# Kernel optimization log

Hardware: AMD Instinct MI355X
Metric: run time of the kernel (lower is better)

Reference implementation:

```python
import jax, jax.numpy as jnp
import numpy as np

N_POINTS = 1440   # number of detector angles (thetas)
N_INT = 4000      # trapezoid integration samples along each ray
N_GRID = 4096     # SoS field is (N_GRID, N_GRID)
GRID_LO, GRID_HI = -0.06, 0.06
R_BODY = 0.05
V0 = 1500.0


def setup_inputs() -> dict:
    key = jax.random.key(0)
    k1, k2, k3 = jax.random.split(key, 3)
    # query point strictly inside the body circle (r < R_body)
    x = jnp.float32(0.012)
    y = jnp.float32(-0.007)
    # speed-of-sound field ~ water SoS with heterogeneity, strictly positive
    SoS = (1480.0 + 40.0 * jax.random.uniform(k3, (N_GRID, N_GRID))).astype(jnp.float32)
    thetas = jnp.linspace(0.0, 2.0 * jnp.pi, N_POINTS, dtype=jnp.float32).reshape(-1, 1)
    steps = jnp.linspace(0.0, 1.0, N_INT, dtype=jnp.float32).reshape(1, -1)
    x_vec = jnp.linspace(GRID_LO, GRID_HI, N_GRID, dtype=jnp.float32)
    dx = x_vec[1] - x_vec[0]
    return {
        "x": x, "y": y, "SoS": SoS,
        "thetas": thetas, "steps": steps,
        "x0": x_vec[0], "y0": x_vec[0], "dx": dx, "dy": dx,
        "R_body": jnp.float32(R_BODY), "v0": jnp.float32(V0),
    }


def reference(x, y, SoS, thetas, steps, x0, y0, dx, dy, R_body, v0):
    # polar coords of query point; note torch code uses atan2(x, y)
    r = jnp.sqrt(x * x + y * y)
    phi = jnp.arctan2(x, y)
    s = r * jnp.sin(thetas - phi)                      # (P,1)
    arg = jnp.maximum(R_body * R_body - s * s, 0.0)    # shared, >0 when r<R_body
    sqrt_arg = jnp.sqrt(arg)
    l_in = sqrt_arg + r * jnp.cos(thetas - phi)
    l_out = 2.0 * sqrt_arg * (jnp.cos(phi - thetas) >= 0.0).astype(sqrt_arg.dtype)
    l = jnp.where(r < R_body, l_in, l_out)             # (P,1) chord lengths

    xs = l * steps                                     # (P,N) arc-length samples
    px = x - xs * jnp.sin(thetas)                      # (P,N) sample positions
    py = y - xs * jnp.cos(thetas)
    x_index = jnp.round((px - x0) / dx).astype(jnp.int32)
    y_index = jnp.round((py - y0) / dy).astype(jnp.int32)
    # gather: negative row index (-y_index) wraps from the end, as in torch/numpy
    vals = 1.0 - v0 / SoS[-y_index, x_index]           # (P,N)
    # trapezoid over non-uniformly labeled x = l*steps (uniform per row)
    dseg = jnp.diff(xs, axis=1)                        # (P,N-1)
    wf = jnp.sum(0.5 * (vals[:, :-1] + vals[:, 1:]) * dseg, axis=1)
    return thetas.reshape(-1), wf
```

## Files before the change

kernel.cpp:

```cpp
#include <hip/hip_runtime.h>

#define N_POINTS 1440
#define N_INT    4000
#define N_GRID   4096
#define BLOCK    256

#define NSEG     8
#define SEG_LEN  (N_INT / NSEG)
#define RPC      4
#define NCLUST   (N_POINTS / RPC)
#define QS       (BLOCK / RPC)
#define FULL_ITS (SEG_LEN / QS)
#define REM_Q    (SEG_LEN - FULL_ITS * QS)

__global__ __launch_bounds__(BLOCK, 8) void wavefront_partial_kernel(
    const float* __restrict__ xp,
    const float* __restrict__ yp,
    const float* __restrict__ SoS,
    const float* __restrict__ thetas,
    const float* __restrict__ x0p,
    const float* __restrict__ y0p,
    const float* __restrict__ dxp,
    const float* __restrict__ dyp,
    const float* __restrict__ Rp,
    const float* __restrict__ v0p,
    float* __restrict__ ws)
{
    const int b = blockIdx.x;
    const int j = b >> 3;
    const int S = ((b & 7) + j) & 7;
    const int t = threadIdx.x;
    const int r = t & 3;
    const int q = t >> 2;

    const int p = j * RPC + r;

    const float x  = xp[0];
    const float y  = yp[0];
    const float x0 = x0p[0];
    const float y0 = y0p[0];
    const float dx = dxp[0];
    const float dy = dyp[0];
    const float Rb = Rp[0];
    const float v0 = v0p[0];

    const float theta = thetas[p];

    const float rr  = sqrtf(x * x + y * y);
    const float phi = atan2f(x, y);
    const float st  = sinf(theta);
    const float ct  = cosf(theta);

    const float sv    = rr * sinf(theta - phi);
    const float arg   = fmaxf(Rb * Rb - sv * sv, 0.0f);
    const float sq    = sqrtf(arg);
    const float l_in  = sq + rr * cosf(theta - phi);
    const float l_out = 2.0f * sq * (cosf(phi - theta) >= 0.0f ? 1.0f : 0.0f);
    const float l     = (rr < Rb) ? l_in : l_out;

    const float ds = 1.0f / 3999.0f;
    const float Ax = (x - x0) / dx;
    const float Bx = l * st / dx;
    const float Ay = (y - y0) / dy;
    const float By = l * ct / dy;

    const int   jb     = S * SEG_LEN + q;
    const float s_base = (float)jb * ds;
    const float fx0  = fmaf(-Bx, s_base, Ax);
    const float fy0  = fmaf(-By, s_base, Ay);
    const float nBxd = -Bx * ((float)QS * ds);
    const float nByd = -By * ((float)QS * ds);

    float acc;

#define SAMPLE(itf, vdst)                                            \
    {                                                                \
        const float fx = fmaf((itf), nBxd, fx0);                     \
        const float fy = fmaf((itf), nByd, fy0);                     \
        const int xi = (int)rintf(fx);                               \
        const int yi = (int)rintf(fy);                               \
        const int idx = ((N_GRID - yi) << 12) + xi;                  \
        const float sosv = SoS[idx];                                 \
        vdst = fmaf(-v0, __builtin_amdgcn_rcpf(sosv), 1.0f);         \
    }

    { float v; SAMPLE(0.0f, v); if (S == 0 && q == 0) v *= 0.5f; acc = v; }
#pragma unroll
    for (int it = 1; it < FULL_ITS; ++it) {
        float v; SAMPLE((float)it, v); acc += v;
    }
    if (q < REM_Q) {
        float v; SAMPLE((float)FULL_ITS, v);
        if (S == NSEG - 1 && q == REM_Q - 1) v *= 0.5f;
        acc += v;
    }
#undef SAMPLE

    acc += __shfl_xor(acc, 4, 64);
    acc += __shfl_xor(acc, 8, 64);
    acc += __shfl_xor(acc, 16, 64);
    acc += __shfl_xor(acc, 32, 64);

    __shared__ float wsum[4][4];
    if ((t & 63) < 4) wsum[t >> 6][r] = acc;
    __syncthreads();
    if (t < 4) {
        const float tot = (wsum[0][t] + wsum[1][t]) + (wsum[2][t] + wsum[3][t]);
        ws[(j * RPC + t) * NSEG + S] = tot;
    }
}

__global__ __launch_bounds__(BLOCK) void wavefront_combine_kernel(
    const float* __restrict__ xp,
    const float* __restrict__ yp,
    const float* __restrict__ thetas,
    const float* __restrict__ Rp,
    const float* __restrict__ ws,
    float* __restrict__ out)
{
    const int p = blockIdx.x * BLOCK + threadIdx.x;
    if (p >= N_POINTS) return;

    const float x  = xp[0];
    const float y  = yp[0];
    const float Rb = Rp[0];
    const float theta = thetas[p];

    const float rr  = sqrtf(x * x + y * y);
    const float phi = atan2f(x, y);
    const float sv    = rr * sinf(theta - phi);
    const float arg   = fmaxf(Rb * Rb - sv * sv, 0.0f);
    const float sq    = sqrtf(arg);
    const float l_in  = sq + rr * cosf(theta - phi);
    const float l_out = 2.0f * sq * (cosf(phi - theta) >= 0.0f ? 1.0f : 0.0f);
    const float l     = (rr < Rb) ? l_in : l_out;

    const float4* w4 = (const float4*)(ws + p * NSEG);
    const float4 a = w4[0], b4 = w4[1];
    const float tot = ((a.x + a.y) + (a.z + a.w)) + ((b4.x + b4.y) + (b4.z + b4.w));

    out[p] = theta;
    out[N_POINTS + p] = l * (1.0f / 3999.0f) * tot;
}

extern "C" void kernel_launch(void* const* d_in, const int* in_sizes, int n_in,
                              void* d_out, int out_size, void* d_ws, size_t ws_size,
                              hipStream_t stream) {
    (void)in_sizes; (void)n_in; (void)out_size; (void)ws_size;

    const float* xp     = (const float*)d_in[0];
    const float* yp     = (const float*)d_in[1];
    const float* SoS    = (const float*)d_in[2];
    const float* thetas = (const float*)d_in[3];
    const float* x0p    = (const float*)d_in[5];
    const float* y0p    = (const float*)d_in[6];
    const float* dxp    = (const float*)d_in[7];
    const float* dyp    = (const float*)d_in[8];
    const float* Rp     = (const float*)d_in[9];
    const float* v0p    = (const float*)d_in[10];

    float* ws  = (float*)d_ws;
    float* out = (float*)d_out;

    wavefront_partial_kernel<<<NCLUST * NSEG, BLOCK, 0, stream>>>(
        xp, yp, SoS, thetas, x0p, y0p, dxp, dyp, Rp, v0p, ws);
    wavefront_combine_kernel<<<(N_POINTS + BLOCK - 1) / BLOCK, BLOCK, 0, stream>>>(
        xp, yp, thetas, Rp, ws, out);
}
```

Baseline: 119.8 us.

## Halve segments, batch gathers before reciprocals, and hoist the v0 multiply

Each block now covers a quarter of a ray instead of an eighth, so each thread issues about 16 gathers. All SoS loads go out first into a register array, and only then are reciprocals taken, which raises memory-level parallelism per thread. Rounding is folded into biased truncation. The 1 - v0/s term is rewritten as n - v0*sum(1/s), with the trapezoid endpoint halving applied as a correction. The trade-off is fewer blocks and more registers (occupancy hint lowered from 8 to 6 blocks), plus slight numeric differences from reassociation and truncation instead of rintf.

```diff
diff --git a/kernel.cpp b/kernel.cpp
--- a/kernel.cpp
+++ b/kernel.cpp
@@ -5,15 +5,14 @@
 #define N_GRID   4096
 #define BLOCK    256
 
-#define NSEG     8
+#define NSEG     4
 #define SEG_LEN  (N_INT / NSEG)
 #define RPC      4
 #define NCLUST   (N_POINTS / RPC)
-#define QS       (BLOCK / RPC)
-#define FULL_ITS (SEG_LEN / QS)
-#define REM_Q    (SEG_LEN - FULL_ITS * QS)
+#define K_FULL   15
+#define TAIL_Q   (SEG_LEN - K_FULL * 64)
 
-__global__ __launch_bounds__(BLOCK, 8) void wavefront_partial_kernel(
+__global__ __launch_bounds__(BLOCK, 6) void wavefront_partial_kernel(
     const float* __restrict__ xp,
     const float* __restrict__ yp,
     const float* __restrict__ SoS,
@@ -27,13 +26,13 @@
     float* __restrict__ ws)
 {
     const int b = blockIdx.x;
-    const int j = b >> 3;
-    const int S = ((b & 7) + j) & 7;
+    const int c = b >> 2;
+    const int S = ((b & 3) + c) & 3;
     const int t = threadIdx.x;
     const int r = t & 3;
     const int q = t >> 2;
 
-    const int p = j * RPC + r;
+    const int p = c * RPC + r;
 
     const float x  = xp[0];
     const float y  = yp[0];
@@ -60,41 +59,50 @@
 
     const float ds = 1.0f / 3999.0f;
     const float Ax = (x - x0) / dx;
-    const float Bx = l * st / dx;
     const float Ay = (y - y0) / dy;
-    const float By = l * ct / dy;
+    const float bx = l * st / dx * ds;
+    const float by = l * ct / dy * ds;
 
-    const int   jb     = S * SEG_LEN + q;
-    const float s_base = (float)jb * ds;
-    const float fx0  = fmaf(-Bx, s_base, Ax);
-    const float fy0  = fmaf(-By, s_base, Ay);
-    const float nBxd = -Bx * ((float)QS * ds);
-    const float nByd = -By * ((float)QS * ds);
+    const int   jb  = S * SEG_LEN + q;
+    const float fx0 = fmaf(-bx, (float)jb, Ax + 0.5f);
+    const float gy0 = fmaf( by, (float)jb, 4096.5f - Ay);
+    const float dX  = -bx * 64.0f;
+    const float dY  =  by * 64.0f;
 
-    float acc;
+    const bool has_tail = (q < TAIL_Q);
 
-#define SAMPLE(itf, vdst)                                            \
-    {                                                                \
-        const float fx = fmaf((itf), nBxd, fx0);                     \
-        const float fy = fmaf((itf), nByd, fy0);                     \
-        const int xi = (int)rintf(fx);                               \
-        const int yi = (int)rintf(fy);                               \
-        const int idx = ((N_GRID - yi) << 12) + xi;                  \
-        const float sosv = SoS[idx];                                 \
-        vdst = fmaf(-v0, __builtin_amdgcn_rcpf(sosv), 1.0f);         \
+    float rv[16];
+#pragma unroll
+    for (int k = 0; k < K_FULL; ++k) {
+        const float kf = (float)k;
+        const int xi  = (int)fmaf(kf, dX, fx0);
+        const int row = (int)fmaf(kf, dY, gy0);
+        rv[k] = SoS[(row << 12) + xi];
+    }
+    if (has_tail) {
+        const float kf = (float)K_FULL;
+        const int xi  = (int)fmaf(kf, dX, fx0);
+        const int row = (int)fmaf(kf, dY, gy0);
+        rv[15] = SoS[(row << 12) + xi];
     }
 
-    { float v; SAMPLE(0.0f, v); if (S == 0 && q == 0) v *= 0.5f; acc = v; }
+    float accR = 0.0f;
 #pragma unroll
-    for (int it = 1; it < FULL_ITS; ++it) {
-        float v; SAMPLE((float)it, v); acc += v;
+    for (int k = 0; k < K_FULL; ++k)
+        accR += __builtin_amdgcn_rcpf(rv[k]);
+    float n = 15.0f;
+    if (has_tail) { accR += __builtin_amdgcn_rcpf(rv[15]); n = 16.0f; }
+
+    if (S == 0 && q == 0) {
+        accR -= 0.5f * __builtin_amdgcn_rcpf(rv[0]);
+        n -= 0.5f;
     }
-    if (q < REM_Q) {
-        float v; SAMPLE((float)FULL_ITS, v);
-        if (S == NSEG - 1 && q == REM_Q - 1) v *= 0.5f;
-        acc += v;
+    if (S == NSEG - 1 && q == TAIL_Q - 1) {
+        accR -= 0.5f * __builtin_amdgcn_rcpf(rv[15]);
+        n -= 0.5f;
     }
-#undef SAMPLE
+
+    float acc = fmaf(-v0, accR, n);
 
     acc += __shfl_xor(acc, 4, 64);
     acc += __shfl_xor(acc, 8, 64);
@@ -106,7 +114,7 @@
     __syncthreads();
     if (t < 4) {
         const float tot = (wsum[0][t] + wsum[1][t]) + (wsum[2][t] + wsum[3][t]);
-        ws[(j * RPC + t) * NSEG + S] = tot;
+        ws[(c * RPC + t) * NSEG + S] = tot;
     }
 }
 
@@ -135,9 +143,8 @@
     const float l_out = 2.0f * sq * (cosf(phi - theta) >= 0.0f ? 1.0f : 0.0f);
     const float l     = (rr < Rb) ? l_in : l_out;
 
-    const float4* w4 = (const float4*)(ws + p * NSEG);
-    const float4 a = w4[0], b4 = w4[1];
-    const float tot = ((a.x + a.y) + (a.z + a.w)) + ((b4.x + b4.y) + (b4.z + b4.w));
+    const float4 a = *(const float4*)(ws + p * NSEG);
+    const float tot = (a.x + a.y) + (a.z + a.w);
 
     out[p] = theta;
     out[N_POINTS + p] = l * (1.0f / 3999.0f) * tot;
```

Result: no change. 117.6 us, median of 2 (-1.9%).
